# Kernel tuning notes

Hardware: AMD Instinct MI355X
Metric: run time of the kernel (lower is better)

Reference implementation:

```python
import jax, jax.numpy as jnp
import numpy as np

DIM = 1024
HEADS = 16
DIM_HEAD = 64


def setup_inputs() -> dict:
    key = jax.random.key(0)
    ks = jax.random.split(key, 6)
    inner = HEADS * DIM_HEAD  # 1024
    s = lambda fan_in: 1.0 / np.sqrt(fan_in)
    return {
        "x": jax.random.normal(ks[0], (4, 4096, DIM), dtype=jnp.float32),
        # weights stored as (in, out): y = x @ W (+ b), equivalent to torch Linear
        "W_qkv": jax.random.normal(ks[1], (DIM, inner * 3), dtype=jnp.float32) * s(DIM),
        "W_f": jax.random.normal(ks[2], (DIM_HEAD, DIM_HEAD), dtype=jnp.float32) * s(DIM_HEAD),
        "b_f": jax.random.normal(ks[3], (DIM_HEAD,), dtype=jnp.float32) * 0.01,
        "W_out": jax.random.normal(ks[4], (inner, DIM), dtype=jnp.float32) * s(inner),
        "b_out": jax.random.normal(ks[5], (DIM,), dtype=jnp.float32) * 0.01,
    }


def reference(x, W_qkv, W_f, b_f, W_out, b_out):
    B, N, C = x.shape
    H, D = HEADS, DIM_HEAD
    qkv = x @ W_qkv  # [B, N, 3*H*D]
    q, k, v = jnp.split(qkv, 3, axis=-1)
    # [B, N, H*D] -> [B, H, N, D]
    reshape = lambda t: t.reshape(B, N, H, D).transpose(0, 2, 1, 3)
    q, k, v = reshape(q), reshape(k), reshape(v)
    # shared feature map: Linear + ReLU applied per-head-dim
    fmap = lambda t: jax.nn.relu(t @ W_f + b_f)
    q = fmap(q)
    k = fmap(k)
    # KV summarization: O(N * D^2)
    kv = jnp.einsum('bhnd,bhne->bhde', k, v)       # [B, H, D, D]
    out = jnp.einsum('bhnd,bhde->bhne', q, kv)     # [B, H, N, D]
    # normalizer: q . sum_n k  (sum over sequence dim)
    k_sum = k.sum(axis=2)                          # [B, H, D]
    normalizer = jnp.einsum('bhnd,bhd->bhn', q, k_sum)
    out = out / (normalizer[..., None] + 1e-6)
    out = out.transpose(0, 2, 1, 3).reshape(B, N, H * D)
    return out @ W_out + b_out
```

## Files before the change

kernel.cpp:

```cpp
#include <hip/hip_runtime.h>
#include <hip/hip_bf16.h>
#include <stdint.h>

#define HEADS 16
#define DHEAD 64
#define DIM   1024
#define SEQ   4096
#define BATCH 4
#define MROWS (BATCH * SEQ)
#define NQKV  (3 * DIM)

typedef short  s16x8 __attribute__((ext_vector_type(8)));
typedef short  s16x4 __attribute__((ext_vector_type(4)));
typedef float  f32x4 __attribute__((ext_vector_type(4)));
typedef unsigned short u16;

__device__ __forceinline__ u16 f2bf(float f) {
  union { float f; uint32_t u; } v; v.f = f;
  uint32_t r = v.u + 0x7fffu + ((v.u >> 16) & 1u);
  return (u16)(r >> 16);
}
__device__ __forceinline__ float bf2f(u16 h) {
  union { uint32_t u; float f; } v; v.u = ((uint32_t)h) << 16;
  return v.f;
}

__device__ __forceinline__ void gload_lds16(const void* g, void* l) {
  __builtin_amdgcn_global_load_lds((__attribute__((address_space(1))) void*)(g),
                                   (__attribute__((address_space(3))) void*)(l),
                                   16, 0, 0);
}

__global__ __launch_bounds__(256) void cast_f32_bf16(const float* __restrict__ src,
                                                     u16* __restrict__ dst, int n) {
  int i = (blockIdx.x * 256 + threadIdx.x) * 4;
  const int stride = gridDim.x * 256 * 4;
  for (; i < n; i += stride) {
    float4 f = *(const float4*)(src + i);
    ushort4 o;
    o.x = f2bf(f.x); o.y = f2bf(f.y); o.z = f2bf(f.z); o.w = f2bf(f.w);
    *(ushort4*)(dst + i) = o;
  }
}

__global__ __launch_bounds__(256) void fold_qk(const float* __restrict__ Wqkv,
                                               const float* __restrict__ Wf,
                                               u16* __restrict__ WqkvT) {
  const int rh  = blockIdx.x >> 3;
  const int kc  = (blockIdx.x & 7) << 7;
  const int reg = rh >> 4, h = rh & 15;
  const int base = reg * DIM + h * DHEAD;
  __shared__ float wc[128 * 64];
  const int tid = threadIdx.x;
  const int j  = tid & 63;
  const int kg = tid >> 6;
  for (int i = tid; i < 128 * 16; i += 256) {
    const int r = i >> 4, c4 = (i & 15) << 2;
    *(float4*)&wc[r * 64 + c4] = *(const float4*)&Wqkv[(size_t)(kc + r) * NQKV + base + c4];
  }
  float v[64];
#pragma unroll
  for (int d = 0; d < 64; d++) v[d] = Wf[d * 64 + j];
  __syncthreads();
  u16* dst = WqkvT + (size_t)(base + j) * DIM + kc + kg * 32;
  for (int ki = 0; ki < 32; ki++) {
    const int k = kg * 32 + ki;
    float s = 0.f;
#pragma unroll
    for (int d = 0; d < 64; d++) s += wc[k * 64 + d] * v[d];
    dst[ki] = f2bf(s);
  }
}

__global__ __launch_bounds__(256) void transpose_cast(const float* __restrict__ src,
                                                      int srcStride, int colOff,
                                                      u16* __restrict__ dst, int Nt) {
  __shared__ float t[64][65];
  const int ntiles = Nt >> 6;
  const int n0 = (blockIdx.x % ntiles) * 64;
  const int k0 = (blockIdx.x / ntiles) * 64;
  for (int i = threadIdx.x; i < 4096; i += 256) {
    const int r = i >> 6, c = i & 63;
    t[r][c] = src[(size_t)(k0 + r) * srcStride + colOff + n0 + c];
  }
  __syncthreads();
  for (int i = threadIdx.x; i < 4096; i += 256) {
    const int r = i & 63, c = i >> 6;
    dst[(size_t)(n0 + c) * DIM + k0 + r] = f2bf(t[r][c]);
  }
}

template <int EPI>
__global__ __launch_bounds__(512, 2) void gemm4p(const u16* __restrict__ A,
                                                 const u16* __restrict__ Bt,
                                                 void* __restrict__ Cout,
                                                 const float* __restrict__ bias,
                                                 int Nn, int K) {
  __shared__ __align__(16) u16 smem[2][2][2][128 * 64];
  const int tilesN = Nn >> 8;
  const int cpx   = gridDim.x >> 3;
  const int xcd   = blockIdx.x & 7;
  const int local = blockIdx.x >> 3;
  const int bmPerX = cpx / tilesN;
  const int perG = 4 * tilesN;
  const int g = local / perG, rrm = local % perG;
  const int bm = xcd * bmPerX + g * 4 + rrm / tilesN;
  const int bn = rrm % tilesN;
  const int m0 = bm << 8, n0 = bn << 8;

  const int tid  = threadIdx.x;
  const int lane = tid & 63;
  const int w    = tid >> 6;
  const int wr = w >> 2, wcn = w & 3;
  const int lrow = lane & 15;
  const int hi   = lane >> 4;
  const int sx   = lrow & 7;

  const int srow  = tid >> 3;
  const int pslot = tid & 7;
  const int gk    = (pslot ^ (srow & 7)) << 3;
  const u16* aBase = A  + (size_t)m0 * K + gk;
  const u16* bBase = Bt + (size_t)n0 * K + gk;

#define STG(buf, op, half, kt, gb)                                             \
  { const u16* s0_ = (gb) + (size_t)((half) * 128 + srow) * K + (kt) * 64;     \
    char* d0_ = (char*)&smem[buf][op][half][0] + tid * 16;                     \
    gload_lds16(s0_, d0_);                                                     \
    gload_lds16(s0_ + (size_t)64 * K, d0_ + 8192); }

#define RDA(buf, dst, mbase)                                                   \
  _Pragma("unroll") for (int mi_ = 0; mi_ < 4; mi_++)                          \
  _Pragma("unroll") for (int kk_ = 0; kk_ < 2; kk_++) {                        \
    const int r_ = ((mbase) + mi_) * 16 + lrow;                                \
    dst[mi_][kk_] = *(const s16x8*)&smem[buf][0][wr]                           \
                        [r_ * 64 + ((kk_ * 4 + hi) ^ sx) * 8]; }

#define RDB(buf, dst, nbase)                                                   \
  _Pragma("unroll") for (int nj_ = 0; nj_ < 2; nj_++)                          \
  _Pragma("unroll") for (int kk_ = 0; kk_ < 2; kk_++) {                        \
    const int r_ = (wcn & 1) * 64 + ((nbase) + nj_) * 16 + lrow;               \
    dst[nj_][kk_] = *(const s16x8*)&smem[buf][1][wcn >> 1]                     \
                        [r_ * 64 + ((kk_ * 4 + hi) ^ sx) * 8]; }

#define MM(mbase, nbase, areg, breg)                                           \
  _Pragma("unroll") for (int mi_ = 0; mi_ < 4; mi_++)                          \
  _Pragma("unroll") for (int nj_ = 0; nj_ < 2; nj_++)                          \
  _Pragma("unroll") for (int kk_ = 0; kk_ < 2; kk_++)                          \
    acc[(mbase) + mi_][(nbase) + nj_] = __builtin_amdgcn_mfma_f32_16x16x32_bf16( \
        breg[nj_][kk_], areg[mi_][kk_], acc[(mbase) + mi_][(nbase) + nj_], 0, 0, 0);

#define WLG  asm volatile("s_waitcnt lgkmcnt(0)" ::: "memory")
#define WVM8 asm volatile("s_waitcnt vmcnt(8)" ::: "memory")
#define WVM4 asm volatile("s_waitcnt vmcnt(4)" ::: "memory")
#define WVM0 asm volatile("s_waitcnt vmcnt(0)" ::: "memory")
#define BAR  __builtin_amdgcn_s_barrier()
#define PRIO1 __builtin_amdgcn_s_setprio(1)
#define PRIO0 __builtin_amdgcn_s_setprio(0)

  f32x4 acc[8][4] = {};
  const int NT  = K >> 6;
  const int NIT = NT >> 1;

  STG(0, 0, 0, 0, aBase); STG(0, 0, 1, 0, aBase);
  STG(0, 1, 0, 0, bBase); STG(0, 1, 1, 0, bBase);
  STG(1, 0, 0, 1, aBase); STG(1, 0, 1, 1, aBase);
  STG(1, 1, 0, 1, bBase); STG(1, 1, 1, 1, bBase);
  WVM8; BAR;

  for (int it = 0; it < NIT; ++it) {
    const int tE = 2 * it + 2, tO = 2 * it + 3;
    const bool pf = (tE < NT);
    s16x8 a[4][2], bl[2][2], bh[2][2];
    RDA(0, a, 0); RDB(0, bl, 0); RDB(0, bh, 2);
    if (it > 0) { STG(1, 0, 0, 2 * it + 1, aBase); STG(1, 0, 1, 2 * it + 1, aBase); }
    BAR; WLG;
    PRIO1; MM(0, 0, a, bl); MM(0, 2, a, bh); PRIO0;
    BAR;
    RDA(0, a, 4);
    if (pf) { STG(0, 1, 0, tE, bBase); STG(0, 1, 1, tE, bBase); }
    BAR;
    if (pf) { WVM4; } else { WVM0; }
    WLG;
    PRIO1; MM(4, 0, a, bl); MM(4, 2, a, bh); PRIO0;
    BAR;
    RDA(1, a, 0); RDB(1, bl, 0); RDB(1, bh, 2);
    if (pf) { STG(0, 0, 0, tE, aBase); STG(0, 0, 1, tE, aBase); }
    BAR; WLG;
    PRIO1; MM(0, 0, a, bl); MM(0, 2, a, bh); PRIO0;
    BAR;
    RDA(1, a, 4);
    if (pf) { STG(1, 1, 0, tO, bBase); STG(1, 1, 1, tO, bBase); }
    BAR;
    if (pf) { WVM4; } else { WVM0; }
    WLG;
    PRIO1; MM(4, 0, a, bl); MM(4, 2, a, bh); PRIO0;
    BAR;
  }

  const int mrow = m0 + wr * 128 + lrow;
  const int nb0  = n0 + wcn * 64 + (hi << 2);
#pragma unroll
  for (int mi = 0; mi < 8; mi++) {
    const int row = mrow + mi * 16;
#pragma unroll
    for (int nj = 0; nj < 4; nj++) {
      const int nb = nb0 + nj * 16;
      float v0 = acc[mi][nj][0], v1 = acc[mi][nj][1];
      float v2 = acc[mi][nj][2], v3 = acc[mi][nj][3];
      if (EPI == 1) {
        if (nb < 2 * DIM) {
          const int bb = nb & 63;
          v0 += bias[bb];     v1 += bias[bb + 1];
          v2 += bias[bb + 2]; v3 += bias[bb + 3];
          v0 = v0 > 0.f ? v0 : 0.f;  v1 = v1 > 0.f ? v1 : 0.f;
          v2 = v2 > 0.f ? v2 : 0.f;  v3 = v3 > 0.f ? v3 : 0.f;
        }
        uint2 st;
        st.x = (uint32_t)f2bf(v0) | ((uint32_t)f2bf(v1) << 16);
        st.y = (uint32_t)f2bf(v2) | ((uint32_t)f2bf(v3) << 16);
        *(uint2*)((u16*)Cout + (size_t)row * Nn + nb) = st;
      } else {
        float4 st;
        st.x = v0 + bias[nb];     st.y = v1 + bias[nb + 1];
        st.z = v2 + bias[nb + 2]; st.w = v3 + bias[nb + 3];
        *(float4*)((float*)Cout + (size_t)row * Nn + nb) = st;
      }
    }
  }
#undef STG
#undef RDA
#undef RDB
#undef MM
#undef WLG
#undef WVM8
#undef WVM4
#undef WVM0
#undef BAR
#undef PRIO1
#undef PRIO0
}

__global__ __launch_bounds__(256) void kv_ksum_mfma(const u16* __restrict__ qkv,
                                                    float* __restrict__ kvpart,
                                                    float* __restrict__ kspart) {
  const int bh = blockIdx.x >> 3;
  const int chunk = blockIdx.x & 7;
  const int b = bh >> 4, h = bh & 15;
  __shared__ u16 kT[64 * 64];
  __shared__ u16 vT[80 * 64];
  const int tid  = threadIdx.x;
  const int lane = tid & 63;
  const int w    = tid >> 6;
  const int lrow = lane & 15;
  const int hi   = lane >> 4;

  for (int i = tid; i < 16 * 64; i += 256) {
    const int r = 64 + (i >> 6), n = i & 63;
    vT[r * 64 + (((n >> 3) ^ (r & 7)) << 3) + (n & 7)] = (r == 64) ? (u16)0x3F80 : (u16)0;
  }

  f32x4 acc[5] = {};
  const u16* kbase = qkv + (size_t)(b * SEQ) * NQKV + DIM     + h * DHEAD;
  const u16* vbase = qkv + (size_t)(b * SEQ) * NQKV + 2 * DIM + h * DHEAD;

  for (int r0 = chunk * 512; r0 < chunk * 512 + 512; r0 += 64) {
    __syncthreads();
    for (int s = tid; s < 512; s += 256) {
      const int r  = s >> 3;
      const int c0 = (s & 7) << 3;
      const s16x8 k8 = *(const s16x8*)(kbase + (size_t)(r0 + r) * NQKV + c0);
      const s16x8 v8 = *(const s16x8*)(vbase + (size_t)(r0 + r) * NQKV + c0);
      const int slot = r >> 3, nb = r & 7;
#pragma unroll
      for (int q = 0; q < 8; q++) {
        const int d = c0 + q;
        const int off = d * 64 + ((slot ^ (d & 7)) << 3) + nb;
        kT[off] = (u16)k8[q];
        vT[off] = (u16)v8[q];
      }
    }
    __syncthreads();
#pragma unroll
    for (int kk = 0; kk < 2; kk++) {
      const int drow = w * 16 + lrow;
      const s16x8 kf = *(const s16x8*)&kT[drow * 64 + (((kk * 4 + hi) ^ (drow & 7)) << 3)];
#pragma unroll
      for (int et = 0; et < 5; et++) {
        const int erow = et * 16 + lrow;
        const s16x8 vf = *(const s16x8*)&vT[erow * 64 + (((kk * 4 + hi) ^ (erow & 7)) << 3)];
        acc[et] = __builtin_amdgcn_mfma_f32_16x16x32_bf16(vf, kf, acc[et], 0, 0, 0);
      }
    }
  }

  const int d = w * 16 + lrow;
  float* outp = kvpart + (size_t)blockIdx.x * 4096;
#pragma unroll
  for (int et = 0; et < 4; et++)
    *(f32x4*)&outp[d * 64 + et * 16 + hi * 4] = acc[et];
  if (hi == 0) kspart[(size_t)blockIdx.x * 64 + d] = acc[4][0];
}

__global__ __launch_bounds__(256) void reduce_kv(const float* __restrict__ kvpart,
                                                 const float* __restrict__ kspart,
                                                 float* __restrict__ kvbuf,
                                                 float* __restrict__ ksumb) {
  const int idx = blockIdx.x * 256 + threadIdx.x;
  if (idx < 64 * 4096) {
    const int bh = idx >> 12, i = idx & 4095;
    float s = 0.f;
#pragma unroll
    for (int c = 0; c < 8; c++) s += kvpart[(size_t)((bh << 3) + c) * 4096 + i];
    kvbuf[idx] = s;
  } else {
    const int idx2 = idx - 64 * 4096;
    if (idx2 < 4096) {
      const int bh = idx2 >> 6, i = idx2 & 63;
      float s = 0.f;
#pragma unroll
      for (int c = 0; c < 8; c++) s += kspart[((bh << 3) + c) * 64 + i];
      ksumb[idx2] = s;
    }
  }
}

__global__ __launch_bounds__(256) void attn_mfma(const u16* __restrict__ qkv,
                                                 const float* __restrict__ kvbuf,
                                                 const float* __restrict__ ksumb,
                                                 u16* __restrict__ attn) {
  const int bh = blockIdx.x >> 4;
  const int mc = blockIdx.x & 15;
  const int b = bh >> 4, h = bh & 15;
  __shared__ u16 BT[2][80][64];
  __shared__ float nrm[256];
  const int tid  = threadIdx.x;
  const int lane = tid & 63;
  const int w    = tid >> 6;
  const int lrow = lane & 15;
  const int hi   = lane >> 4;

#pragma unroll
  for (int s = 0; s < 20; s++) {
    const int idx = tid + 256 * s;
    const int e = idx >> 6, d = idx & 63;
    float v;
    if (e < 64)       v = kvbuf[(size_t)bh * 4096 + d * 64 + e];
    else if (e == 64) v = ksumb[bh * 64 + d];
    else              v = 0.f;
    const u16 vh = f2bf(v);
    const u16 vl = f2bf(v - bf2f(vh));
    const int off = e * 64 + (((d >> 3) ^ (e & 7)) << 3) + (d & 7);
    BT[0][0][off] = vh;
    BT[1][0][off] = vl;
  }

  const int rloc = w * 64 + lrow;
  const u16* qbase = qkv + (size_t)(b * SEQ + mc * 256 + rloc) * NQKV + h * DHEAD + hi * 8;
  s16x8 af[4][2];
#pragma unroll
  for (int mi = 0; mi < 4; mi++)
#pragma unroll
    for (int kk = 0; kk < 2; kk++)
      af[mi][kk] = *(const s16x8*)(qbase + (size_t)(mi * 16) * NQKV + kk * 32);

  __syncthreads();

  f32x4 acc[4][5] = {};
#pragma unroll
  for (int wv = 0; wv < 2; wv++) {
#pragma unroll
    for (int jb = 0; jb < 5; jb++) {
      const int erow = jb * 16 + lrow;
      const int sx = erow & 7;
      s16x8 bq0 = *(const s16x8*)&BT[wv][erow][((0 * 4 + hi) ^ sx) << 3];
      s16x8 bq1 = *(const s16x8*)&BT[wv][erow][((1 * 4 + hi) ^ sx) << 3];
#pragma unroll
      for (int mi = 0; mi < 4; mi++) {
        acc[mi][jb] = __builtin_amdgcn_mfma_f32_16x16x32_bf16(bq0, af[mi][0], acc[mi][jb], 0, 0, 0);
        acc[mi][jb] = __builtin_amdgcn_mfma_f32_16x16x32_bf16(bq1, af[mi][1], acc[mi][jb], 0, 0, 0);
      }
    }
  }

  if (hi == 0) {
#pragma unroll
    for (int mi = 0; mi < 4; mi++) nrm[rloc + mi * 16] = acc[mi][4][0] + 1e-6f;
  }
  __syncthreads();

  u16* obase = attn + (size_t)(b * SEQ + mc * 256 + rloc) * DIM + h * DHEAD + hi * 4;
#pragma unroll
  for (int mi = 0; mi < 4; mi++) {
    const float sc = 1.f / nrm[rloc + mi * 16];
#pragma unroll
    for (int jb = 0; jb < 4; jb++) {
      uint2 st;
      st.x = (uint32_t)f2bf(acc[mi][jb][0] * sc) | ((uint32_t)f2bf(acc[mi][jb][1] * sc) << 16);
      st.y = (uint32_t)f2bf(acc[mi][jb][2] * sc) | ((uint32_t)f2bf(acc[mi][jb][3] * sc) << 16);
      *(uint2*)(obase + (size_t)(mi * 16) * DIM + jb * 16) = st;
    }
  }
}

extern "C" void kernel_launch(void* const* d_in, const int* in_sizes, int n_in,
                              void* d_out, int out_size, void* d_ws, size_t ws_size,
                              hipStream_t stream) {
  (void)in_sizes; (void)n_in; (void)out_size; (void)ws_size;
  const float* x     = (const float*)d_in[0];
  const float* Wqkv  = (const float*)d_in[1];
  const float* Wf    = (const float*)d_in[2];
  const float* bfv   = (const float*)d_in[3];
  const float* Wout  = (const float*)d_in[4];
  const float* bout  = (const float*)d_in[5];
  float* out = (float*)d_out;
  char* ws = (char*)d_ws;

  u16*   wqkvT = (u16*)(ws + 0);
  u16*   woutT = (u16*)(ws + 6291456);
  u16*   xb    = (u16*)(ws + 8388608);
  u16*   qkvb  = (u16*)(ws + 41943040);
  u16*   attn  = (u16*)(ws + 142606336);
  float* kvp   = (float*)(ws + 176160768);
  float* ksp   = (float*)(ws + 184549376);
  float* kvbuf = (float*)(ws + 184680448);
  float* ksumb = (float*)(ws + 185729024);

  cast_f32_bf16<<<2048, 256, 0, stream>>>(x, xb, MROWS * DIM);
  fold_qk<<<256, 256, 0, stream>>>(Wqkv, Wf, wqkvT);
  transpose_cast<<<256, 256, 0, stream>>>(Wqkv, NQKV, 2 * DIM, wqkvT + (size_t)2 * DIM * DIM, DIM);
  transpose_cast<<<256, 256, 0, stream>>>(Wout, DIM, 0, woutT, DIM);
  gemm4p<1><<<(MROWS / 256) * (NQKV / 256), 512, 0, stream>>>(xb, wqkvT, qkvb, bfv,
                                                              NQKV, DIM);
  kv_ksum_mfma<<<64 * 8, 256, 0, stream>>>(qkvb, kvp, ksp);
  reduce_kv<<<(64 * 4096 + 64 * 64 + 255) / 256, 256, 0, stream>>>(kvp, ksp, kvbuf, ksumb);
  attn_mfma<<<64 * 16, 256, 0, stream>>>(qkvb, kvbuf, ksumb, attn);
  gemm4p<2><<<(MROWS / 256) * (DIM / 256), 512, 0, stream>>>(attn, woutT, out, bout,
                                                             DIM, DIM);
}
```

Measured before the change: 257.0 us.

## Fuse fp32-to-bf16 cast of x into QKV GEMM A-operand load path

```diff
diff --git a/kernel.cpp b/kernel.cpp
--- a/kernel.cpp
+++ b/kernel.cpp
@@ -29,18 +29,6 @@
   __builtin_amdgcn_global_load_lds((__attribute__((address_space(1))) void*)(g),
                                    (__attribute__((address_space(3))) void*)(l),
                                    16, 0, 0);
-}
-
-__global__ __launch_bounds__(256) void cast_f32_bf16(const float* __restrict__ src,
-                                                     u16* __restrict__ dst, int n) {
-  int i = (blockIdx.x * 256 + threadIdx.x) * 4;
-  const int stride = gridDim.x * 256 * 4;
-  for (; i < n; i += stride) {
-    float4 f = *(const float4*)(src + i);
-    ushort4 o;
-    o.x = f2bf(f.x); o.y = f2bf(f.y); o.z = f2bf(f.z); o.w = f2bf(f.w);
-    *(ushort4*)(dst + i) = o;
-  }
 }
 
 __global__ __launch_bounds__(256) void fold_qk(const float* __restrict__ Wqkv,
@@ -90,8 +78,9 @@
   }
 }
 
-template <int EPI>
-__global__ __launch_bounds__(512, 2) void gemm4p(const u16* __restrict__ A,
+template <int EPI, int AF32>
+__global__ __launch_bounds__(512, 2) void gemm4p(const float* __restrict__ Af,
+                                                 const u16* __restrict__ Ab,
                                                  const u16* __restrict__ Bt,
                                                  void* __restrict__ Cout,
                                                  const float* __restrict__ bias,
@@ -119,7 +108,7 @@
   const int srow  = tid >> 3;
   const int pslot = tid & 7;
   const int gk    = (pslot ^ (srow & 7)) << 3;
-  const u16* aBase = A  + (size_t)m0 * K + gk;
+  const u16* aBase = Ab + (size_t)m0 * K + gk;
   const u16* bBase = Bt + (size_t)n0 * K + gk;
 
 #define STG(buf, op, half, kt, gb)                                             \
@@ -127,6 +116,29 @@
     char* d0_ = (char*)&smem[buf][op][half][0] + tid * 16;                     \
     gload_lds16(s0_, d0_);                                                     \
     gload_lds16(s0_ + (size_t)64 * K, d0_ + 8192); }
+
+#define AISSUE(dst, kt)                                                        \
+  _Pragma("unroll") for (int h_ = 0; h_ < 2; h_++)                             \
+  _Pragma("unroll") for (int rr_ = 0; rr_ < 2; rr_++) {                        \
+    const float* s_ = Af + (size_t)(m0 + h_ * 128 + srow + rr_ * 64) * K       \
+                      + (kt) * 64 + pslot * 8;                                 \
+    dst[h_ * 4 + rr_ * 2]     = *(const float4*)(s_);                          \
+    dst[h_ * 4 + rr_ * 2 + 1] = *(const float4*)(s_ + 4);                      \
+  }
+
+#define AWRITE(buf, src)                                                       \
+  _Pragma("unroll") for (int h_ = 0; h_ < 2; h_++)                             \
+  _Pragma("unroll") for (int rr_ = 0; rr_ < 2; rr_++) {                        \
+    const float4 f0_ = src[h_ * 4 + rr_ * 2];                                  \
+    const float4 f1_ = src[h_ * 4 + rr_ * 2 + 1];                              \
+    s16x8 p_;                                                                  \
+    p_[0] = (short)f2bf(f0_.x); p_[1] = (short)f2bf(f0_.y);                    \
+    p_[2] = (short)f2bf(f0_.z); p_[3] = (short)f2bf(f0_.w);                    \
+    p_[4] = (short)f2bf(f1_.x); p_[5] = (short)f2bf(f1_.y);                    \
+    p_[6] = (short)f2bf(f1_.z); p_[7] = (short)f2bf(f1_.w);                    \
+    *(s16x8*)((char*)&smem[buf][0][h_][0]                                      \
+        + (size_t)(srow + rr_ * 64) * 128 + ((pslot ^ (srow & 7)) << 4)) = p_; \
+  }
 
 #define RDA(buf, dst, mbase)                                                   \
   _Pragma("unroll") for (int mi_ = 0; mi_ < 4; mi_++)                          \
@@ -149,11 +161,12 @@
     acc[(mbase) + mi_][(nbase) + nj_] = __builtin_amdgcn_mfma_f32_16x16x32_bf16( \
         breg[nj_][kk_], areg[mi_][kk_], acc[(mbase) + mi_][(nbase) + nj_], 0, 0, 0);
 
-#define WLG  asm volatile("s_waitcnt lgkmcnt(0)" ::: "memory")
-#define WVM8 asm volatile("s_waitcnt vmcnt(8)" ::: "memory")
-#define WVM4 asm volatile("s_waitcnt vmcnt(4)" ::: "memory")
-#define WVM0 asm volatile("s_waitcnt vmcnt(0)" ::: "memory")
-#define BAR  __builtin_amdgcn_s_barrier()
+#define WLG   asm volatile("s_waitcnt lgkmcnt(0)" ::: "memory")
+#define WVM16 asm volatile("s_waitcnt vmcnt(16)" ::: "memory")
+#define WVM8  asm volatile("s_waitcnt vmcnt(8)" ::: "memory")
+#define WVM4  asm volatile("s_waitcnt vmcnt(4)" ::: "memory")
+#define WVM0  asm volatile("s_waitcnt vmcnt(0)" ::: "memory")
+#define BAR   __builtin_amdgcn_s_barrier()
 #define PRIO1 __builtin_amdgcn_s_setprio(1)
 #define PRIO0 __builtin_amdgcn_s_setprio(0)
 
@@ -161,40 +174,78 @@
   const int NT  = K >> 6;
   const int NIT = NT >> 1;
 
-  STG(0, 0, 0, 0, aBase); STG(0, 0, 1, 0, aBase);
-  STG(0, 1, 0, 0, bBase); STG(0, 1, 1, 0, bBase);
-  STG(1, 0, 0, 1, aBase); STG(1, 0, 1, 1, aBase);
-  STG(1, 1, 0, 1, bBase); STG(1, 1, 1, 1, bBase);
-  WVM8; BAR;
-
-  for (int it = 0; it < NIT; ++it) {
-    const int tE = 2 * it + 2, tO = 2 * it + 3;
-    const bool pf = (tE < NT);
-    s16x8 a[4][2], bl[2][2], bh[2][2];
-    RDA(0, a, 0); RDB(0, bl, 0); RDB(0, bh, 2);
-    if (it > 0) { STG(1, 0, 0, 2 * it + 1, aBase); STG(1, 0, 1, 2 * it + 1, aBase); }
-    BAR; WLG;
-    PRIO1; MM(0, 0, a, bl); MM(0, 2, a, bh); PRIO0;
-    BAR;
-    RDA(0, a, 4);
-    if (pf) { STG(0, 1, 0, tE, bBase); STG(0, 1, 1, tE, bBase); }
-    BAR;
-    if (pf) { WVM4; } else { WVM0; }
-    WLG;
-    PRIO1; MM(4, 0, a, bl); MM(4, 2, a, bh); PRIO0;
-    BAR;
-    RDA(1, a, 0); RDB(1, bl, 0); RDB(1, bh, 2);
-    if (pf) { STG(0, 0, 0, tE, aBase); STG(0, 0, 1, tE, aBase); }
-    BAR; WLG;
-    PRIO1; MM(0, 0, a, bl); MM(0, 2, a, bh); PRIO0;
-    BAR;
-    RDA(1, a, 4);
-    if (pf) { STG(1, 1, 0, tO, bBase); STG(1, 1, 1, tO, bBase); }
-    BAR;
-    if (pf) { WVM4; } else { WVM0; }
-    WLG;
-    PRIO1; MM(4, 0, a, bl); MM(4, 2, a, bh); PRIO0;
-    BAR;
+  if constexpr (AF32) {
+    float4 aldE[8], aldO[8];
+    AISSUE(aldE, 0);
+    AISSUE(aldO, 1);
+    STG(0, 1, 0, 0, bBase); STG(0, 1, 1, 0, bBase);
+    STG(1, 1, 0, 1, bBase); STG(1, 1, 1, 1, bBase);
+    WVM16;
+    AWRITE(0, aldE);
+    WLG; BAR;
+
+    for (int it = 0; it < NIT; ++it) {
+      const int tE = 2 * it + 2, tO = 2 * it + 3;
+      const bool pf = (tE < NT);
+      s16x8 a[4][2], bl[2][2], bh[2][2];
+      WVM4;
+      AWRITE(1, aldO);
+      RDA(0, a, 0); RDB(0, bl, 0); RDB(0, bh, 2);
+      BAR; WLG;
+      PRIO1; MM(0, 0, a, bl); MM(0, 2, a, bh); PRIO0;
+      BAR;
+      if (pf) { AISSUE(aldE, tE); STG(0, 1, 0, tE, bBase); STG(0, 1, 1, tE, bBase); }
+      RDA(0, a, 4);
+      BAR; WLG;
+      PRIO1; MM(4, 0, a, bl); MM(4, 2, a, bh); PRIO0;
+      BAR;
+      if (pf) { WVM4; AWRITE(0, aldE); } else { WVM0; }
+      RDA(1, a, 0); RDB(1, bl, 0); RDB(1, bh, 2);
+      BAR; WLG;
+      PRIO1; MM(0, 0, a, bl); MM(0, 2, a, bh); PRIO0;
+      BAR;
+      if (pf) { AISSUE(aldO, tO); STG(1, 1, 0, tO, bBase); STG(1, 1, 1, tO, bBase); }
+      RDA(1, a, 4);
+      BAR; WLG;
+      PRIO1; MM(4, 0, a, bl); MM(4, 2, a, bh); PRIO0;
+      BAR;
+    }
+  } else {
+    STG(0, 0, 0, 0, aBase); STG(0, 0, 1, 0, aBase);
+    STG(0, 1, 0, 0, bBase); STG(0, 1, 1, 0, bBase);
+    STG(1, 0, 0, 1, aBase); STG(1, 0, 1, 1, aBase);
+    STG(1, 1, 0, 1, bBase); STG(1, 1, 1, 1, bBase);
+    WVM8; BAR;
+
+    for (int it = 0; it < NIT; ++it) {
+      const int tE = 2 * it + 2, tO = 2 * it + 3;
+      const bool pf = (tE < NT);
+      s16x8 a[4][2], bl[2][2], bh[2][2];
+      RDA(0, a, 0); RDB(0, bl, 0); RDB(0, bh, 2);
+      if (it > 0) { STG(1, 0, 0, 2 * it + 1, aBase); STG(1, 0, 1, 2 * it + 1, aBase); }
+      BAR; WLG;
+      PRIO1; MM(0, 0, a, bl); MM(0, 2, a, bh); PRIO0;
+      BAR;
+      RDA(0, a, 4);
+      if (pf) { STG(0, 1, 0, tE, bBase); STG(0, 1, 1, tE, bBase); }
+      BAR;
+      if (pf) { WVM4; } else { WVM0; }
+      WLG;
+      PRIO1; MM(4, 0, a, bl); MM(4, 2, a, bh); PRIO0;
+      BAR;
+      RDA(1, a, 0); RDB(1, bl, 0); RDB(1, bh, 2);
+      if (pf) { STG(0, 0, 0, tE, aBase); STG(0, 0, 1, tE, aBase); }
+      BAR; WLG;
+      PRIO1; MM(0, 0, a, bl); MM(0, 2, a, bh); PRIO0;
+      BAR;
+      RDA(1, a, 4);
+      if (pf) { STG(1, 1, 0, tO, bBase); STG(1, 1, 1, tO, bBase); }
+      BAR;
+      if (pf) { WVM4; } else { WVM0; }
+      WLG;
+      PRIO1; MM(4, 0, a, bl); MM(4, 2, a, bh); PRIO0;
+      BAR;
+    }
   }
 
   const int mrow = m0 + wr * 128 + lrow;
@@ -228,10 +279,13 @@
     }
   }
 #undef STG
+#undef AISSUE
+#undef AWRITE
 #undef RDA
 #undef RDB
 #undef MM
 #undef WLG
+#undef WVM16
 #undef WVM8
 #undef WVM4
 #undef WVM0
@@ -417,7 +471,6 @@
 
   u16*   wqkvT = (u16*)(ws + 0);
   u16*   woutT = (u16*)(ws + 6291456);
-  u16*   xb    = (u16*)(ws + 8388608);
   u16*   qkvb  = (u16*)(ws + 41943040);
   u16*   attn  = (u16*)(ws + 142606336);
   float* kvp   = (float*)(ws + 176160768);
@@ -425,15 +478,14 @@
   float* kvbuf = (float*)(ws + 184680448);
   float* ksumb = (float*)(ws + 185729024);
 
-  cast_f32_bf16<<<2048, 256, 0, stream>>>(x, xb, MROWS * DIM);
   fold_qk<<<256, 256, 0, stream>>>(Wqkv, Wf, wqkvT);
   transpose_cast<<<256, 256, 0, stream>>>(Wqkv, NQKV, 2 * DIM, wqkvT + (size_t)2 * DIM * DIM, DIM);
   transpose_cast<<<256, 256, 0, stream>>>(Wout, DIM, 0, woutT, DIM);
-  gemm4p<1><<<(MROWS / 256) * (NQKV / 256), 512, 0, stream>>>(xb, wqkvT, qkvb, bfv,
-                                                              NQKV, DIM);
+  gemm4p<1, 1><<<(MROWS / 256) * (NQKV / 256), 512, 0, stream>>>(
+      x, (const u16*)x, wqkvT, qkvb, bfv, NQKV, DIM);
   kv_ksum_mfma<<<64 * 8, 256, 0, stream>>>(qkvb, kvp, ksp);
   reduce_kv<<<(64 * 4096 + 64 * 64 + 255) / 256, 256, 0, stream>>>(kvp, ksp, kvbuf, ksumb);
   attn_mfma<<<64 * 16, 256, 0, stream>>>(qkvb, kvbuf, ksumb, attn);
-  gemm4p<2><<<(MROWS / 256) * (DIM / 256), 512, 0, stream>>>(attn, woutT, out, bout,
-                                                             DIM, DIM);
-}
+  gemm4p<2, 0><<<(MROWS / 256) * (DIM / 256), 512, 0, stream>>>(
+      nullptr, attn, woutT, out, bout, DIM, DIM);
+}
```

Result: slower. 505.5 us (+96.7%).
